# Performance work log

Measured on AMD Instinct MI355X. Metric: run time of the kernel, lower is better.

The kernel has to match this reference:

```python
import jax, jax.numpy as jnp
import numpy as np

N = 50000   # nodes
E = 500000  # edges
G = 64      # graphs in batch
H = 2       # attention heads
D = 64      # hidden per head (hid)
F_IN = 4    # num_features
C = 5       # num_classes
NEG_SLOPE = 0.2


def setup_inputs() -> dict:
    key = jax.random.key(0)
    ks = jax.random.split(key, 24)
    inp = {
        'x': jax.random.normal(ks[0], (N, F_IN), jnp.float32),
        'edge_index': jax.random.randint(ks[1], (2, E), 0, N, dtype=jnp.int64),
        'batch': jnp.sort(jax.random.randint(ks[2], (N,), 0, G, dtype=jnp.int64)),
    }
    ins = [F_IN, H * D, H * D, H * D]
    ki = 3
    for l, fin in enumerate(ins, 1):
        s = 1.0 / np.sqrt(fin)
        inp[f'W{l}'] = s * jax.random.normal(ks[ki], (fin, H * D), jnp.float32); ki += 1
        inp[f'asrc{l}'] = 0.1 * jax.random.normal(ks[ki], (H, D), jnp.float32); ki += 1
        inp[f'adst{l}'] = 0.1 * jax.random.normal(ks[ki], (H, D), jnp.float32); ki += 1
        inp[f'b{l}'] = 0.01 * jax.random.normal(ks[ki], (H * D,), jnp.float32); ki += 1
    inp['lin_w'] = (1.0 / np.sqrt(H * D)) * jax.random.normal(ks[ki], (H * D, C), jnp.float32); ki += 1
    inp['lin_b'] = jnp.zeros((C,), jnp.float32)
    return inp


def gat_conv(x, src, dst, W, a_src, a_dst, b):
    # x: [N, Fin] -> h: [N, H, D]
    h = (x @ W).reshape(-1, H, D)
    alpha_src = jnp.sum(h * a_src, axis=-1)  # [N, H]
    alpha_dst = jnp.sum(h * a_dst, axis=-1)  # [N, H]
    e = jax.nn.leaky_relu(alpha_src[src] + alpha_dst[dst], NEG_SLOPE)  # [E, H]
    # segment softmax over incoming edges of each dst node
    e_max = jax.ops.segment_max(e, dst, num_segments=N)  # [N, H]
    e_exp = jnp.exp(e - e_max[dst])
    denom = jax.ops.segment_sum(e_exp, dst, num_segments=N)
    alpha = e_exp / (denom[dst] + 1e-16)  # [E, H]
    msg = h[src] * alpha[:, :, None]  # [E, H, D]
    out = jax.ops.segment_sum(msg, dst, num_segments=N)  # [N, H, D]
    return out.reshape(-1, H * D) + b


def reference(x, edge_index, batch,
              W1, asrc1, adst1, b1,
              W2, asrc2, adst2, b2,
              W3, asrc3, adst3, b3,
              W4, asrc4, adst4, b4,
              lin_w, lin_b):
    src, dst = edge_index[0], edge_index[1]
    h = jax.nn.relu(gat_conv(x, src, dst, W1, asrc1, adst1, b1))
    h = jax.nn.relu(gat_conv(h, src, dst, W2, asrc2, adst2, b2))
    h = jax.nn.relu(gat_conv(h, src, dst, W3, asrc3, adst3, b3))
    h = jax.nn.relu(gat_conv(h, src, dst, W4, asrc4, adst4, b4))
    # global mean pool over graphs
    sums = jax.ops.segment_sum(h, batch, num_segments=G)  # [G, 128]
    counts = jax.ops.segment_sum(jnp.ones((h.shape[0],), h.dtype), batch, num_segments=G)
    pooled = sums / jnp.maximum(counts, 1.0)[:, None]
    return jax.nn.sigmoid(pooled @ lin_w + lin_b)  # [G, C]
```

## Files before the change

kernel.cpp:

```cpp
#include <hip/hip_runtime.h>
#include <math.h>

#define NHEAD 2
#define NDIM  64
#define HD    128
#define NGRAPH 64
#define NCLS  5
#define NEG_SLOPE 0.2f

typedef __attribute__((ext_vector_type(8))) short bf16x8;
typedef __attribute__((ext_vector_type(4))) float f32x4;

static __device__ __forceinline__ unsigned short f2bf(float f) {
    unsigned int u = __float_as_uint(f);
    u = (u + 0x7fff + ((u >> 16) & 1)) >> 16;
    return (unsigned short)u;
}
static __device__ __forceinline__ float bf2f(unsigned short b) {
    return __uint_as_float((unsigned int)b << 16);
}


__global__ void k_deg(const int* __restrict__ dst, int* __restrict__ deg, int E) {
    int i = blockIdx.x * blockDim.x + threadIdx.x;
    if (i < E) atomicAdd(&deg[dst[i]], 1);
}

__global__ __launch_bounds__(256) void k_scan_local(const int* __restrict__ deg,
                                                    int* __restrict__ ptr,
                                                    int* __restrict__ bsum, int n) {
    __shared__ int wsum[4];
    const int tid = threadIdx.x, lane = tid & 63, wid = tid >> 6;
    const int base = blockIdx.x * 2048 + tid * 8;
    int v[8];
    #pragma unroll
    for (int k = 0; k < 8; ++k) {
        int i = base + k;
        v[k] = (i < n) ? deg[i] : 0;
    }
    #pragma unroll
    for (int k = 1; k < 8; ++k) v[k] += v[k - 1];
    int x = v[7];
    #pragma unroll
    for (int off = 1; off < 64; off <<= 1) {
        int t = __shfl_up(x, off, 64);
        if (lane >= off) x += t;
    }
    if (lane == 63) wsum[wid] = x;
    __syncthreads();
    int woff = 0;
    #pragma unroll
    for (int k = 0; k < 4; ++k) woff += (k < wid) ? wsum[k] : 0;
    int texcl = woff + x - v[7];
    #pragma unroll
    for (int k = 0; k < 8; ++k) {
        int i = base + k;
        if (i < n) ptr[i + 1] = texcl + v[k];
    }
    if (tid == 255) bsum[blockIdx.x] = woff + x;
    if (blockIdx.x == 0 && tid == 0) ptr[0] = 0;
}

__global__ void k_scan_bsum(int* __restrict__ bsum, int B) {
    int lane = threadIdx.x;
    int carry = 0;
    for (int base = 0; base < B; base += 64) {
        int i = base + lane;
        int v = (i < B) ? bsum[i] : 0;
        int x = v;
        #pragma unroll
        for (int off = 1; off < 64; off <<= 1) {
            int t = __shfl_up(x, off, 64);
            if (lane >= off) x += t;
        }
        if (i < B) bsum[i] = carry + x - v;
        carry += __shfl(x, 63, 64);
    }
}

__global__ __launch_bounds__(256) void k_scan_add(int* __restrict__ ptr,
                                                  const int* __restrict__ bsum, int n) {
    int off = bsum[blockIdx.x];
    if (off == 0) return;
    const int base = blockIdx.x * 2048 + threadIdx.x * 8;
    #pragma unroll
    for (int k = 0; k < 8; ++k) {
        int i = base + k;
        if (i < n) ptr[i + 1] += off;
    }
}

__global__ void k_scatter(const int* __restrict__ src, const int* __restrict__ dst,
                          const int* __restrict__ ptr, int* __restrict__ fill,
                          int* __restrict__ csr, int E) {
    int i = blockIdx.x * blockDim.x + threadIdx.x;
    if (i < E) {
        int d = dst[i];
        int pos = atomicAdd(&fill[d], 1);
        csr[ptr[d] + pos] = src[i];
    }
}


__global__ void k_prepw(const float* __restrict__ W2, const float* __restrict__ W3,
                        const float* __restrict__ W4, unsigned short* __restrict__ Wt) {
    int idx = blockIdx.x * blockDim.x + threadIdx.x;
    if (idx >= 3 * HD * HD) return;
    int l = idx / (HD * HD), rem = idx % (HD * HD);
    int n = rem >> 7, k = rem & 127;
    const float* W = (l == 0) ? W2 : (l == 1) ? W3 : W4;
    Wt[idx] = f2bf(W[k * HD + n]);
}

__global__ void k_gemm1_alpha(const float* __restrict__ x, const float* __restrict__ W,
                              const float* __restrict__ asrc, const float* __restrict__ adst,
                              unsigned short* __restrict__ out, float* __restrict__ oas,
                              float* __restrict__ oad, int N) {
    int n = (blockIdx.x * blockDim.x + threadIdx.x) >> 6;
    int lane = threadIdx.x & 63;
    if (n >= N) return;
    float4 xv = *(const float4*)&x[n * 4];
    int c0 = lane * 2;
    float2 w0 = *(const float2*)&W[c0];
    float2 w1 = *(const float2*)&W[128 + c0];
    float2 w2 = *(const float2*)&W[256 + c0];
    float2 w3 = *(const float2*)&W[384 + c0];
    float v0 = xv.x * w0.x + xv.y * w1.x + xv.z * w2.x + xv.w * w3.x;
    float v1 = xv.x * w0.y + xv.y * w1.y + xv.z * w2.y + xv.w * w3.y;
    unsigned short b0 = f2bf(v0), b1 = f2bf(v1);
    unsigned int packed = (unsigned int)b0 | ((unsigned int)b1 << 16);
    *(unsigned int*)&out[(size_t)n * HD + c0] = packed;
    float vx = bf2f(b0), vy = bf2f(b1);
    float2 av = *(const float2*)&asrc[c0];
    float2 dv = *(const float2*)&adst[c0];
    float s = vx * av.x + vy * av.y;
    float t = vx * dv.x + vy * dv.y;
    #pragma unroll
    for (int off = 16; off > 0; off >>= 1) {
        s += __shfl_xor(s, off);
        t += __shfl_xor(t, off);
    }
    if ((lane & 31) == 0) {
        int head = lane >> 5;
        oas[n * 2 + head] = s;
        oad[n * 2 + head] = t;
    }
}

#define LDA 136
__global__ __launch_bounds__(256) void k_gemm_mfma(const unsigned short* __restrict__ A,
                                                   const unsigned short* __restrict__ Wt,
                                                   const float* __restrict__ asrc,
                                                   const float* __restrict__ adst,
                                                   unsigned short* __restrict__ out,
                                                   float* __restrict__ oas,
                                                   float* __restrict__ oad, int N) {
    __shared__ unsigned short As[128 * LDA];
    __shared__ unsigned short Ws[128 * LDA];
    const int tid = threadIdx.x;
    const int nbase = blockIdx.x * 128;
    const int lane = tid & 63, w = tid >> 6;
    const int l15 = lane & 15, quad = lane >> 4;
    const int koff = quad * 8;

    for (int c = tid; c < 2048; c += 256) {
        int row = c >> 4, k8 = (c & 15) << 3;
        int g = nbase + row;
        uint4 v = make_uint4(0, 0, 0, 0);
        if (g < N) v = *(const uint4*)&A[(size_t)g * HD + k8];
        *(uint4*)&As[row * LDA + k8] = v;
    }
    for (int c = tid; c < 2048; c += 256) {
        int row = c >> 4, k8 = (c & 15) << 3;
        *(uint4*)&Ws[row * LDA + k8] = *(const uint4*)&Wt[row * HD + k8];
    }
    float av[8], dv[8];
    #pragma unroll
    for (int c = 0; c < 8; ++c) {
        av[c] = asrc[c * 16 + l15];
        dv[c] = adst[c * 16 + l15];
    }
    __syncthreads();

    f32x4 acc0[8], acc1[8];
    #pragma unroll
    for (int c = 0; c < 8; ++c) { acc0[c] = (f32x4)(0.f); acc1[c] = (f32x4)(0.f); }

    const int r0 = w * 32 + l15;
    #pragma unroll
    for (int ks = 0; ks < 4; ++ks) {
        bf16x8 a0 = *(const bf16x8*)&As[r0 * LDA + ks * 32 + koff];
        bf16x8 a1 = *(const bf16x8*)&As[(r0 + 16) * LDA + ks * 32 + koff];
        #pragma unroll
        for (int c = 0; c < 8; ++c) {
            bf16x8 b = *(const bf16x8*)&Ws[(c * 16 + l15) * LDA + ks * 32 + koff];
            acc0[c] = __builtin_amdgcn_mfma_f32_16x16x32_bf16(a0, b, acc0[c], 0, 0, 0);
            acc1[c] = __builtin_amdgcn_mfma_f32_16x16x32_bf16(a1, b, acc1[c], 0, 0, 0);
        }
    }

    #pragma unroll
    for (int i = 0; i < 2; ++i) {
        int rowb = nbase + w * 32 + i * 16 + quad * 4;
        #pragma unroll
        for (int c = 0; c < 8; ++c) {
            f32x4 v = i ? acc1[c] : acc0[c];
            int col = c * 16 + l15;
            #pragma unroll
            for (int r = 0; r < 4; ++r) {
                int row = rowb + r;
                if (row < N) out[(size_t)row * HD + col] = f2bf(v[r]);
            }
        }
        #pragma unroll
        for (int r = 0; r < 4; ++r) {
            float ps0 = 0.f, ps1 = 0.f, pd0 = 0.f, pd1 = 0.f;
            #pragma unroll
            for (int c = 0; c < 4; ++c) {
                float hv = i ? acc1[c][r] : acc0[c][r];
                ps0 += hv * av[c]; pd0 += hv * dv[c];
            }
            #pragma unroll
            for (int c = 4; c < 8; ++c) {
                float hv = i ? acc1[c][r] : acc0[c][r];
                ps1 += hv * av[c]; pd1 += hv * dv[c];
            }
            #pragma unroll
            for (int off = 1; off < 16; off <<= 1) {
                ps0 += __shfl_xor(ps0, off);
                ps1 += __shfl_xor(ps1, off);
                pd0 += __shfl_xor(pd0, off);
                pd1 += __shfl_xor(pd1, off);
            }
            int row = rowb + r;
            if (l15 == 0 && row < N) {
                *(float2*)&oas[row * 2] = make_float2(ps0, ps1);
                *(float2*)&oad[row * 2] = make_float2(pd0, pd1);
            }
        }
    }
}

__global__ void k_agg(const unsigned short* __restrict__ h, const float* __restrict__ oas,
                      const float* __restrict__ oad, const int* __restrict__ ptr,
                      const int* __restrict__ csr, const float* __restrict__ bias,
                      unsigned short* __restrict__ out, int N) {
    int n = (blockIdx.x * blockDim.x + threadIdx.x) >> 6;
    int lane = threadIdx.x & 63;
    if (n >= N) return;
    int beg = ptr[n], end = ptr[n + 1];
    if (beg == end) {
        float2 b2 = *(const float2*)&bias[lane * 2];
        unsigned int packed = (unsigned int)f2bf(fmaxf(b2.x, 0.f)) |
                              ((unsigned int)f2bf(fmaxf(b2.y, 0.f)) << 16);
        *(unsigned int*)&out[(size_t)n * HD + lane * 2] = packed;
        return;
    }
    const int quad = lane >> 4, sub = lane & 15;
    const int hsel = sub >> 3;
    float2 adn = *(const float2*)&oad[n * 2];
    float m0 = -INFINITY, m1 = -INFINITY, l0 = 0.f, l1 = 0.f;
    float acc[8];
    #pragma unroll
    for (int k = 0; k < 8; ++k) acc[k] = 0.f;

    auto accum = [&](uint4 hv, float pj) {
        #pragma unroll
        for (int k = 0; k < 4; ++k) {
            unsigned int u = (&hv.x)[k];
            acc[2 * k]     += pj * __uint_as_float(u << 16);
            acc[2 * k + 1] += pj * __uint_as_float(u & 0xffff0000u);
        }
    };

    for (int cbeg = beg; cbeg < end; cbeg += 64) {
        int cnt = min(64, end - cbeg);
        int ng = (cnt + 3) >> 2;
        int s = 0;
        if (lane < cnt) s = csr[cbeg + lane];

        int sjA = __shfl(s, quad);
        uint4 hA = *(const uint4*)&h[(size_t)sjA * HD + sub * 8];
        uint4 hB = make_uint4(0, 0, 0, 0);
        if (ng > 1) {
            int sjB = __shfl(s, 4 + quad);
            hB = *(const uint4*)&h[(size_t)sjB * HD + sub * 8];
        }

        float e0 = -INFINITY, e1 = -INFINITY;
        if (lane < cnt) {
            float2 as = *(const float2*)&oas[s * 2];
            e0 = as.x + adn.x; e0 = (e0 >= 0.f) ? e0 : NEG_SLOPE * e0;
            e1 = as.y + adn.y; e1 = (e1 >= 0.f) ? e1 : NEG_SLOPE * e1;
        }
        float c0 = e0, c1 = e1;
        #pragma unroll
        for (int off = 32; off > 0; off >>= 1) {
            c0 = fmaxf(c0, __shfl_xor(c0, off));
            c1 = fmaxf(c1, __shfl_xor(c1, off));
        }
        float nm0 = fmaxf(m0, c0), nm1 = fmaxf(m1, c1);
        float sc0 = __expf(m0 - nm0), sc1 = __expf(m1 - nm1);
        float p0 = (lane < cnt) ? __expf(e0 - nm0) : 0.f;
        float p1 = (lane < cnt) ? __expf(e1 - nm1) : 0.f;
        float s0 = p0, s1 = p1;
        #pragma unroll
        for (int off = 32; off > 0; off >>= 1) {
            s0 += __shfl_xor(s0, off);
            s1 += __shfl_xor(s1, off);
        }
        l0 = l0 * sc0 + s0;
        l1 = l1 * sc1 + s1;
        m0 = nm0; m1 = nm1;
        float scl = hsel ? sc1 : sc0;
        #pragma unroll
        for (int k = 0; k < 8; ++k) acc[k] *= scl;

        float paA = __shfl(p0, quad),     pbA = __shfl(p1, quad);
        float pA  = hsel ? pbA : paA;
        float pB = 0.f;
        if (ng > 1) {
            float paB = __shfl(p0, 4 + quad), pbB = __shfl(p1, 4 + quad);
            pB = hsel ? pbB : paB;
        }
        for (int g = 2; g < ng; ++g) {
            int jq = g * 4 + quad;
            int sjC = __shfl(s, jq);
            float paC = __shfl(p0, jq), pbC = __shfl(p1, jq);
            float pC  = hsel ? pbC : paC;
            uint4 hC = *(const uint4*)&h[(size_t)sjC * HD + sub * 8];
            accum(hA, pA);
            hA = hB; pA = pB;
            hB = hC; pB = pC;
        }
        accum(hA, pA);
        if (ng > 1) accum(hB, pB);
    }
    #pragma unroll
    for (int k = 0; k < 8; ++k) {
        acc[k] += __shfl_xor(acc[k], 16);
        acc[k] += __shfl_xor(acc[k], 32);
    }
    if (quad == 0) {
        float lsel = hsel ? l1 : l0;
        float inv = 1.f / (lsel + 1e-16f);
        float4 ba = *(const float4*)&bias[sub * 8];
        float4 bb = *(const float4*)&bias[sub * 8 + 4];
        float o[8];
        o[0] = fmaxf(acc[0] * inv + ba.x, 0.f);
        o[1] = fmaxf(acc[1] * inv + ba.y, 0.f);
        o[2] = fmaxf(acc[2] * inv + ba.z, 0.f);
        o[3] = fmaxf(acc[3] * inv + ba.w, 0.f);
        o[4] = fmaxf(acc[4] * inv + bb.x, 0.f);
        o[5] = fmaxf(acc[5] * inv + bb.y, 0.f);
        o[6] = fmaxf(acc[6] * inv + bb.z, 0.f);
        o[7] = fmaxf(acc[7] * inv + bb.w, 0.f);
        uint4 pk;
        pk.x = (unsigned int)f2bf(o[0]) | ((unsigned int)f2bf(o[1]) << 16);
        pk.y = (unsigned int)f2bf(o[2]) | ((unsigned int)f2bf(o[3]) << 16);
        pk.z = (unsigned int)f2bf(o[4]) | ((unsigned int)f2bf(o[5]) << 16);
        pk.w = (unsigned int)f2bf(o[6]) | ((unsigned int)f2bf(o[7]) << 16);
        *(uint4*)&out[(size_t)n * HD + sub * 8] = pk;
    }
}

__global__ void k_pool(const unsigned short* __restrict__ feat, const int* __restrict__ batch,
                       float* __restrict__ pooled, int* __restrict__ gcount, int N) {
    int col = threadIdx.x;
    int n0 = blockIdx.x * 128;
    int n1 = min(n0 + 128, N);
    float acc = 0.f;
    int curg = -1, runlen = 0;
    for (int n = n0; n < n1; ++n) {
        int g = batch[n];
        if (g != curg) {
            if (curg >= 0) {
                atomicAdd(&pooled[curg * HD + col], acc);
                if (col == 0) atomicAdd(&gcount[curg], runlen);
            }
            acc = 0.f; runlen = 0;
            curg = g;
        }
        acc += bf2f(feat[(size_t)n * HD + col]);
        runlen++;
    }
    if (curg >= 0) {
        atomicAdd(&pooled[curg * HD + col], acc);
        if (col == 0) atomicAdd(&gcount[curg], runlen);
    }
}

__global__ void k_final(const float* __restrict__ pooled, const int* __restrict__ gcount,
                        const float* __restrict__ lw, const float* __restrict__ lb,
                        float* __restrict__ out) {
    int tid = threadIdx.x;
    if (tid >= NGRAPH * NCLS) return;
    int g = tid / NCLS, c = tid % NCLS;
    float cnt = fmaxf((float)gcount[g], 1.f);
    const float* p = pooled + g * HD;
    float sum = 0.f;
    for (int k = 0; k < HD; ++k)
        sum += p[k] * lw[k * NCLS + c];
    float z = lb[c] + sum / cnt;
    out[tid] = 1.f / (1.f + __expf(-z));
}


static inline size_t al256(size_t x) { return (x + 255) & ~(size_t)255; }

extern "C" void kernel_launch(void* const* d_in, const int* in_sizes, int n_in,
                              void* d_out, int out_size, void* d_ws, size_t ws_size,
                              hipStream_t stream) {
    const int N = in_sizes[0] / 4;
    const int E = in_sizes[1] / 2;

    const float* x     = (const float*)d_in[0];
    const int*   esrc  = (const int*)d_in[1];
    const int*   edst  = esrc + E;
    const int*   batch = (const int*)d_in[2];
    const float* Wl[4]  = {(const float*)d_in[3],  (const float*)d_in[7],
                           (const float*)d_in[11], (const float*)d_in[15]};
    const float* asr[4] = {(const float*)d_in[4],  (const float*)d_in[8],
                           (const float*)d_in[12], (const float*)d_in[16]};
    const float* ads[4] = {(const float*)d_in[5],  (const float*)d_in[9],
                           (const float*)d_in[13], (const float*)d_in[17]};
    const float* bs[4]  = {(const float*)d_in[6],  (const float*)d_in[10],
                           (const float*)d_in[14], (const float*)d_in[18]};
    const float* lin_w = (const float*)d_in[19];
    const float* lin_b = (const float*)d_in[20];
    float* out = (float*)d_out;

    char* w = (char*)d_ws;
    size_t off = 0;
    auto alloc = [&](size_t bytes) -> void* {
        void* p = w + off;
        off = al256(off + bytes);
        return p;
    };
    int*   deg    = (int*)alloc((size_t)N * 4);
    int*   fill   = (int*)alloc((size_t)N * 4);
    int*   gcount = (int*)alloc((size_t)NGRAPH * 4);
    float* pooled = (float*)alloc((size_t)NGRAPH * HD * 4);
    size_t zbytes = off;
    int*   ptr    = (int*)alloc((size_t)(N + 1) * 4);
    int*   bsum   = (int*)alloc((size_t)1024 * 4);
    int*   csr    = (int*)alloc((size_t)E * 4);
    unsigned short* hbuf = (unsigned short*)alloc((size_t)N * HD * 2);
    unsigned short* feat = (unsigned short*)alloc((size_t)N * HD * 2);
    unsigned short* Wt   = (unsigned short*)alloc((size_t)3 * HD * HD * 2);
    float* a_src  = (float*)alloc((size_t)N * 2 * 4);
    float* a_dst  = (float*)alloc((size_t)N * 2 * 4);
    (void)ws_size; (void)n_in; (void)out_size;

    hipMemsetAsync(d_ws, 0, zbytes, stream);

    k_prepw<<<(3 * HD * HD + 255) / 256, 256, 0, stream>>>(Wl[1], Wl[2], Wl[3], Wt);
    k_deg<<<(E + 255) / 256, 256, 0, stream>>>(edst, deg, E);
    const int SB = (N + 2047) / 2048;
    k_scan_local<<<SB, 256, 0, stream>>>(deg, ptr, bsum, N);
    k_scan_bsum<<<1, 64, 0, stream>>>(bsum, SB);
    k_scan_add<<<SB, 256, 0, stream>>>(ptr, bsum, N);
    k_scatter<<<(E + 255) / 256, 256, 0, stream>>>(esrc, edst, ptr, fill, csr, E);

    const int node_wave_blocks = (N + 3) / 4;

    for (int layer = 0; layer < 4; ++layer) {
        if (layer == 0) {
            k_gemm1_alpha<<<node_wave_blocks, 256, 0, stream>>>(
                x, Wl[0], asr[0], ads[0], hbuf, a_src, a_dst, N);
        } else {
            k_gemm_mfma<<<(N + 127) / 128, 256, 0, stream>>>(
                feat, Wt + (size_t)(layer - 1) * HD * HD,
                asr[layer], ads[layer], hbuf, a_src, a_dst, N);
        }
        k_agg<<<node_wave_blocks, 256, 0, stream>>>(hbuf, a_src, a_dst, ptr, csr, bs[layer], feat, N);
    }

    k_pool<<<(N + 127) / 128, 128, 0, stream>>>(feat, batch, pooled, gcount, N);
    k_final<<<1, 320, 0, stream>>>(pooled, gcount, lin_w, lin_b, out);
}
```

Before: 399.1 us.

## Process four nodes per wavefront in aggregation and drop LDS staging in GEMM

The aggregation kernel now gives each node a 16-lane group instead of a whole wavefront, so four destination nodes share one wave. Each group walks its edge list in chunks of 16 with an online softmax, using shuffles within the group and a wave-wide loop bound taken from the largest group count. This targets idle lanes on low-degree nodes (about 10 average in-degree), at the cost of divergence when degrees within a wave differ. The MFMA GEMM now reads A and W fragments straight from global memory instead of staging them in shared memory, and each block covers 64 rows instead of 128. That removes LDS traffic and the barrier but relies on cache for reuse of W.

```diff
diff --git a/kernel.cpp b/kernel.cpp
--- a/kernel.cpp
+++ b/kernel.cpp
@@ -147,7 +147,6 @@
     }
 }
 
-#define LDA 136
 __global__ __launch_bounds__(256) void k_gemm_mfma(const unsigned short* __restrict__ A,
                                                    const unsigned short* __restrict__ Wt,
                                                    const float* __restrict__ asrc,
@@ -155,110 +154,95 @@
                                                    unsigned short* __restrict__ out,
                                                    float* __restrict__ oas,
                                                    float* __restrict__ oad, int N) {
-    __shared__ unsigned short As[128 * LDA];
-    __shared__ unsigned short Ws[128 * LDA];
     const int tid = threadIdx.x;
-    const int nbase = blockIdx.x * 128;
+    const int nbase = blockIdx.x * 64;
     const int lane = tid & 63, w = tid >> 6;
     const int l15 = lane & 15, quad = lane >> 4;
     const int koff = quad * 8;
 
-    for (int c = tid; c < 2048; c += 256) {
-        int row = c >> 4, k8 = (c & 15) << 3;
-        int g = nbase + row;
-        uint4 v = make_uint4(0, 0, 0, 0);
-        if (g < N) v = *(const uint4*)&A[(size_t)g * HD + k8];
-        *(uint4*)&As[row * LDA + k8] = v;
-    }
-    for (int c = tid; c < 2048; c += 256) {
-        int row = c >> 4, k8 = (c & 15) << 3;
-        *(uint4*)&Ws[row * LDA + k8] = *(const uint4*)&Wt[row * HD + k8];
-    }
     float av[8], dv[8];
     #pragma unroll
     for (int c = 0; c < 8; ++c) {
         av[c] = asrc[c * 16 + l15];
         dv[c] = adst[c * 16 + l15];
     }
-    __syncthreads();
-
-    f32x4 acc0[8], acc1[8];
-    #pragma unroll
-    for (int c = 0; c < 8; ++c) { acc0[c] = (f32x4)(0.f); acc1[c] = (f32x4)(0.f); }
-
-    const int r0 = w * 32 + l15;
+
+    f32x4 acc[8];
+    #pragma unroll
+    for (int c = 0; c < 8; ++c) acc[c] = (f32x4)(0.f);
+
+    const int g0 = nbase + w * 16 + l15;
     #pragma unroll
     for (int ks = 0; ks < 4; ++ks) {
-        bf16x8 a0 = *(const bf16x8*)&As[r0 * LDA + ks * 32 + koff];
-        bf16x8 a1 = *(const bf16x8*)&As[(r0 + 16) * LDA + ks * 32 + koff];
+        bf16x8 a0 = (bf16x8)(short)0;
+        if (g0 < N) a0 = *(const bf16x8*)&A[(size_t)g0 * HD + ks * 32 + koff];
         #pragma unroll
         for (int c = 0; c < 8; ++c) {
-            bf16x8 b = *(const bf16x8*)&Ws[(c * 16 + l15) * LDA + ks * 32 + koff];
-            acc0[c] = __builtin_amdgcn_mfma_f32_16x16x32_bf16(a0, b, acc0[c], 0, 0, 0);
-            acc1[c] = __builtin_amdgcn_mfma_f32_16x16x32_bf16(a1, b, acc1[c], 0, 0, 0);
-        }
-    }
-
-    #pragma unroll
-    for (int i = 0; i < 2; ++i) {
-        int rowb = nbase + w * 32 + i * 16 + quad * 4;
-        #pragma unroll
-        for (int c = 0; c < 8; ++c) {
-            f32x4 v = i ? acc1[c] : acc0[c];
-            int col = c * 16 + l15;
-            #pragma unroll
-            for (int r = 0; r < 4; ++r) {
-                int row = rowb + r;
-                if (row < N) out[(size_t)row * HD + col] = f2bf(v[r]);
-            }
-        }
+            bf16x8 b = *(const bf16x8*)&Wt[(size_t)(c * 16 + l15) * HD + ks * 32 + koff];
+            acc[c] = __builtin_amdgcn_mfma_f32_16x16x32_bf16(a0, b, acc[c], 0, 0, 0);
+        }
+    }
+
+    const int rowb = nbase + w * 16 + quad * 4;
+    #pragma unroll
+    for (int c = 0; c < 8; ++c) {
+        f32x4 v = acc[c];
+        int col = c * 16 + l15;
         #pragma unroll
         for (int r = 0; r < 4; ++r) {
-            float ps0 = 0.f, ps1 = 0.f, pd0 = 0.f, pd1 = 0.f;
-            #pragma unroll
-            for (int c = 0; c < 4; ++c) {
-                float hv = i ? acc1[c][r] : acc0[c][r];
-                ps0 += hv * av[c]; pd0 += hv * dv[c];
-            }
-            #pragma unroll
-            for (int c = 4; c < 8; ++c) {
-                float hv = i ? acc1[c][r] : acc0[c][r];
-                ps1 += hv * av[c]; pd1 += hv * dv[c];
-            }
-            #pragma unroll
-            for (int off = 1; off < 16; off <<= 1) {
-                ps0 += __shfl_xor(ps0, off);
-                ps1 += __shfl_xor(ps1, off);
-                pd0 += __shfl_xor(pd0, off);
-                pd1 += __shfl_xor(pd1, off);
-            }
             int row = rowb + r;
-            if (l15 == 0 && row < N) {
-                *(float2*)&oas[row * 2] = make_float2(ps0, ps1);
-                *(float2*)&oad[row * 2] = make_float2(pd0, pd1);
-            }
-        }
-    }
-}
-
-__global__ void k_agg(const unsigned short* __restrict__ h, const float* __restrict__ oas,
-                      const float* __restrict__ oad, const int* __restrict__ ptr,
-                      const int* __restrict__ csr, const float* __restrict__ bias,
-                      unsigned short* __restrict__ out, int N) {
-    int n = (blockIdx.x * blockDim.x + threadIdx.x) >> 6;
-    int lane = threadIdx.x & 63;
-    if (n >= N) return;
-    int beg = ptr[n], end = ptr[n + 1];
-    if (beg == end) {
-        float2 b2 = *(const float2*)&bias[lane * 2];
-        unsigned int packed = (unsigned int)f2bf(fmaxf(b2.x, 0.f)) |
-                              ((unsigned int)f2bf(fmaxf(b2.y, 0.f)) << 16);
-        *(unsigned int*)&out[(size_t)n * HD + lane * 2] = packed;
-        return;
-    }
-    const int quad = lane >> 4, sub = lane & 15;
+            if (row < N) out[(size_t)row * HD + col] = f2bf(v[r]);
+        }
+    }
+    #pragma unroll
+    for (int r = 0; r < 4; ++r) {
+        float ps0 = 0.f, ps1 = 0.f, pd0 = 0.f, pd1 = 0.f;
+        #pragma unroll
+        for (int c = 0; c < 4; ++c) {
+            float hv = acc[c][r];
+            ps0 += hv * av[c]; pd0 += hv * dv[c];
+        }
+        #pragma unroll
+        for (int c = 4; c < 8; ++c) {
+            float hv = acc[c][r];
+            ps1 += hv * av[c]; pd1 += hv * dv[c];
+        }
+        #pragma unroll
+        for (int off = 1; off < 16; off <<= 1) {
+            ps0 += __shfl_xor(ps0, off);
+            ps1 += __shfl_xor(ps1, off);
+            pd0 += __shfl_xor(pd0, off);
+            pd1 += __shfl_xor(pd1, off);
+        }
+        int row = rowb + r;
+        if (l15 == 0 && row < N) {
+            *(float2*)&oas[row * 2] = make_float2(ps0, ps1);
+            *(float2*)&oad[row * 2] = make_float2(pd0, pd1);
+        }
+    }
+}
+
+__global__ __launch_bounds__(256) void k_agg(const unsigned short* __restrict__ h,
+                                             const float* __restrict__ oas,
+                                             const float* __restrict__ oad,
+                                             const int* __restrict__ ptr,
+                                             const int* __restrict__ csr,
+                                             const float* __restrict__ bias,
+                                             unsigned short* __restrict__ out, int N) {
+    const int tid = threadIdx.x;
+    const int lane = tid & 63;
+    const int grp = lane >> 4, sub = lane & 15;
+    const int gbase = lane & 48;
+    const int n = ((blockIdx.x * blockDim.x + tid) >> 6) * 4 + grp;
     const int hsel = sub >> 3;
-    float2 adn = *(const float2*)&oad[n * 2];
+    const bool valid = (n < N);
+
+    int beg = 0, end = 0;
+    float2 adn = make_float2(0.f, 0.f);
+    if (valid) {
+        beg = ptr[n]; end = ptr[n + 1];
+        adn = *(const float2*)&oad[n * 2];
+    }
     float m0 = -INFINITY, m1 = -INFINITY, l0 = 0.f, l1 = 0.f;
     float acc[8];
     #pragma unroll
@@ -273,39 +257,32 @@
         }
     };
 
-    for (int cbeg = beg; cbeg < end; cbeg += 64) {
-        int cnt = min(64, end - cbeg);
-        int ng = (cnt + 3) >> 2;
+    int cbeg = beg;
+    while (__any(cbeg < end)) {
+        int rem = end - cbeg;
+        int cnt = rem < 0 ? 0 : (rem > 16 ? 16 : rem);
         int s = 0;
-        if (lane < cnt) s = csr[cbeg + lane];
-
-        int sjA = __shfl(s, quad);
-        uint4 hA = *(const uint4*)&h[(size_t)sjA * HD + sub * 8];
-        uint4 hB = make_uint4(0, 0, 0, 0);
-        if (ng > 1) {
-            int sjB = __shfl(s, 4 + quad);
-            hB = *(const uint4*)&h[(size_t)sjB * HD + sub * 8];
-        }
-
         float e0 = -INFINITY, e1 = -INFINITY;
-        if (lane < cnt) {
+        if (sub < cnt) {
+            s = csr[cbeg + sub];
             float2 as = *(const float2*)&oas[s * 2];
             e0 = as.x + adn.x; e0 = (e0 >= 0.f) ? e0 : NEG_SLOPE * e0;
             e1 = as.y + adn.y; e1 = (e1 >= 0.f) ? e1 : NEG_SLOPE * e1;
         }
         float c0 = e0, c1 = e1;
         #pragma unroll
-        for (int off = 32; off > 0; off >>= 1) {
+        for (int off = 8; off > 0; off >>= 1) {
             c0 = fmaxf(c0, __shfl_xor(c0, off));
             c1 = fmaxf(c1, __shfl_xor(c1, off));
         }
         float nm0 = fmaxf(m0, c0), nm1 = fmaxf(m1, c1);
-        float sc0 = __expf(m0 - nm0), sc1 = __expf(m1 - nm1);
-        float p0 = (lane < cnt) ? __expf(e0 - nm0) : 0.f;
-        float p1 = (lane < cnt) ? __expf(e1 - nm1) : 0.f;
+        float sc0 = (nm0 == -INFINITY) ? 0.f : __expf(m0 - nm0);
+        float sc1 = (nm1 == -INFINITY) ? 0.f : __expf(m1 - nm1);
+        float p0 = (sub < cnt) ? __expf(e0 - nm0) : 0.f;
+        float p1 = (sub < cnt) ? __expf(e1 - nm1) : 0.f;
         float s0 = p0, s1 = p1;
         #pragma unroll
-        for (int off = 32; off > 0; off >>= 1) {
+        for (int off = 8; off > 0; off >>= 1) {
             s0 += __shfl_xor(s0, off);
             s1 += __shfl_xor(s1, off);
         }
@@ -316,32 +293,37 @@
         #pragma unroll
         for (int k = 0; k < 8; ++k) acc[k] *= scl;
 
-        float paA = __shfl(p0, quad),     pbA = __shfl(p1, quad);
-        float pA  = hsel ? pbA : paA;
-        float pB = 0.f;
-        if (ng > 1) {
-            float paB = __shfl(p0, 4 + quad), pbB = __shfl(p1, 4 + quad);
-            pB = hsel ? pbB : paB;
-        }
-        for (int g = 2; g < ng; ++g) {
-            int jq = g * 4 + quad;
-            int sjC = __shfl(s, jq);
-            float paC = __shfl(p0, jq), pbC = __shfl(p1, jq);
-            float pC  = hsel ? pbC : paC;
-            uint4 hC = *(const uint4*)&h[(size_t)sjC * HD + sub * 8];
+        int jm = cnt;
+        jm = max(jm, __shfl_xor(jm, 16));
+        jm = max(jm, __shfl_xor(jm, 32));
+
+        auto fetchp = [&](int j, uint4& hv, float& pj) {
+            int sj = __shfl(s, gbase + j);
+            float pa = __shfl(p0, gbase + j);
+            float pb = __shfl(p1, gbase + j);
+            pj = hsel ? pb : pa;
+            hv = make_uint4(0, 0, 0, 0);
+            if (j < cnt)
+                hv = *(const uint4*)&h[(size_t)sj * HD + sub * 8];
+        };
+        uint4 hA, hB = make_uint4(0, 0, 0, 0);
+        float pA, pB = 0.f;
+        fetchp(0, hA, pA);
+        if (jm > 1) fetchp(1, hB, pB);
+        for (int j = 2; j < jm; ++j) {
+            uint4 hC; float pC;
+            fetchp(j, hC, pC);
             accum(hA, pA);
             hA = hB; pA = pB;
             hB = hC; pB = pC;
         }
         accum(hA, pA);
-        if (ng > 1) accum(hB, pB);
-    }
-    #pragma unroll
-    for (int k = 0; k < 8; ++k) {
-        acc[k] += __shfl_xor(acc[k], 16);
-        acc[k] += __shfl_xor(acc[k], 32);
-    }
-    if (quad == 0) {
+        if (jm > 1) accum(hB, pB);
+
+        cbeg += 16;
+    }
+
+    if (valid) {
         float lsel = hsel ? l1 : l0;
         float inv = 1.f / (lsel + 1e-16f);
         float4 ba = *(const float4*)&bias[sub * 8];
@@ -463,17 +445,18 @@
     k_scatter<<<(E + 255) / 256, 256, 0, stream>>>(esrc, edst, ptr, fill, csr, E);
 
     const int node_wave_blocks = (N + 3) / 4;
+    const int agg_blocks = (N + 15) / 16;
 
     for (int layer = 0; layer < 4; ++layer) {
         if (layer == 0) {
             k_gemm1_alpha<<<node_wave_blocks, 256, 0, stream>>>(
                 x, Wl[0], asr[0], ads[0], hbuf, a_src, a_dst, N);
         } else {
-            k_gemm_mfma<<<(N + 127) / 128, 256, 0, stream>>>(
+            k_gemm_mfma<<<(N + 63) / 64, 256, 0, stream>>>(
                 feat, Wt + (size_t)(layer - 1) * HD * HD,
                 asr[layer], ads[layer], hbuf, a_src, a_dst, N);
         }
-        k_agg<<<node_wave_blocks, 256, 0, stream>>>(hbuf, a_src, a_dst, ptr, csr, bs[layer], feat, N);
+        k_agg<<<agg_blocks, 256, 0, stream>>>(hbuf, a_src, a_dst, ptr, csr, bs[layer], feat, N);
     }
 
     k_pool<<<(N + 127) / 128, 128, 0, stream>>>(feat, batch, pooled, gcount, N);
```

Result: no change. 396.1 us (-0.8%).
